# Kernel tuning notes

Hardware: AMD Instinct MI355X
Metric: run time of the kernel (lower is better)

Reference implementation:

```python
import jax, jax.numpy as jnp
import numpy as np

B, S, D = 32, 512, 512
H, DH = 8, 64          # head_num, att_embedding_size
DFF = 4 * D
NEG = float(-2**32 + 1)
LN_EPS = 1e-3          # keras LayerNormalization default


def layer_norm(x, gamma, beta):
    mu = jnp.mean(x, axis=-1, keepdims=True)
    var = jnp.mean(jnp.square(x - mu), axis=-1, keepdims=True)
    return (x - mu) / jnp.sqrt(var + LN_EPS) * gamma + beta


def setup_inputs() -> dict:
    key = jax.random.key(0)
    ks = jax.random.split(key, 10)
    queries = jax.random.normal(ks[0], (B, S, D), dtype=jnp.float32)
    keys = jax.random.normal(ks[1], (B, S, D), dtype=jnp.float32)
    query_lens = jax.random.randint(ks[2], (B, 1), 1, S + 1)
    key_lens = jax.random.randint(ks[3], (B, 1), 1, S + 1)
    # learned params (TruncatedNormal stddev 0.05-ish / Glorot approximated by scaled normals)
    W_Q = jax.random.normal(ks[4], (D, D), dtype=jnp.float32) * 0.05
    W_K = jax.random.normal(ks[5], (D, D), dtype=jnp.float32) * 0.05
    W_V = jax.random.normal(ks[6], (D, D), dtype=jnp.float32) * 0.05
    fw1 = jax.random.normal(ks[7], (D, DFF), dtype=jnp.float32) * (1.0 / np.sqrt(D))
    fw2 = jax.random.normal(ks[8], (DFF, D), dtype=jnp.float32) * (1.0 / np.sqrt(DFF))
    ln_gamma = jnp.ones((D,), dtype=jnp.float32)
    ln_beta = jnp.zeros((D,), dtype=jnp.float32)
    return {"queries": queries, "keys": keys, "W_Q": W_Q, "W_K": W_K, "W_V": W_V,
            "fw1": fw1, "fw2": fw2, "ln_gamma": ln_gamma, "ln_beta": ln_beta,
            "query_lens": query_lens, "key_lens": key_lens}


def reference(queries, keys, W_Q, W_K, W_V, fw1, fw2, ln_gamma, ln_beta, query_lens, key_lens):
    # masks from sequence lengths: [B, S] float {0,1}
    pos = jnp.arange(S)
    q_mask = (pos[None, :] < query_lens).astype(queries.dtype)  # [B,S]
    k_mask = (pos[None, :] < key_lens).astype(queries.dtype)    # [B,S]

    # QKV projections, split into heads: [B,S,H,DH]
    Q = (queries @ W_Q).reshape(B, S, H, DH)
    Kp = (keys @ W_K).reshape(B, S, H, DH)
    V = (keys @ W_V).reshape(B, S, H, DH)

    # scaled dot-product scores: [B,H,Sq,Sk]
    scores = jnp.einsum('bqhd,bkhd->bhqk', Q, Kp) / jnp.sqrt(jnp.asarray(DH, queries.dtype))

    # key padding mask
    scores = jnp.where(k_mask[:, None, None, :] == 1, scores, NEG)
    # blinding: kill the diagonal (self-position)
    eye = jnp.eye(S, dtype=bool)
    scores = jnp.where(eye[None, None, :, :], NEG, scores)

    scores = scores - jnp.max(scores, axis=-1, keepdims=True)
    attn = jax.nn.softmax(scores, axis=-1)
    # query mask zeros out padded query rows (after softmax, as in source)
    attn = attn * q_mask[:, None, :, None]

    out = jnp.einsum('bhqk,bkhd->bqhd', attn, V).reshape(B, S, D)

    result = out + queries                       # use_res
    result = layer_norm(result, ln_gamma, ln_beta)  # shared ln (use_layer_norm)

    # feed-forward
    h = jax.nn.relu(result @ fw1) @ fw2
    result = result + h
    result = layer_norm(result, ln_gamma, ln_beta)

    # output_type == 'mean'
    return jnp.mean(result, axis=1, keepdims=True)  # [B,1,D]
```

## Files before the change

kernel.cpp:

```cpp
#include <hip/hip_runtime.h>

typedef unsigned short ushort_t;
typedef unsigned int uint_t;
typedef __attribute__((ext_vector_type(4))) float f32x4;
typedef __attribute__((ext_vector_type(2))) float f32x2;
typedef __attribute__((ext_vector_type(8))) short s16x8;
typedef __attribute__((ext_vector_type(8))) _Float16 f16x8;
typedef __attribute__((ext_vector_type(4))) unsigned short u16x4;

#define NEGV -60000.0f

__device__ __forceinline__ ushort_t f2bf(float f) {
  unsigned int u = __builtin_bit_cast(unsigned int, f);
  return (ushort_t)((u + 0x7fffu + ((u >> 16) & 1u)) >> 16);
}
__device__ __forceinline__ float bf2f(ushort_t h) {
  unsigned int u = ((unsigned int)h) << 16;
  return __builtin_bit_cast(float, u);
}
__device__ __forceinline__ void gload_lds16(const void* g, void* l) {
  __builtin_amdgcn_global_load_lds(
      (const __attribute__((address_space(1))) unsigned int*)g,
      (__attribute__((address_space(3))) unsigned int*)l, 16, 0, 0);
}

template<int EPI>
__global__ __launch_bounds__(512, 2)
void gemm256(const ushort_t* __restrict__ A, const ushort_t* __restrict__ A2,
             int lda,
             const ushort_t* __restrict__ Bt, int ldb,
             void* __restrict__ Cv, int ldc, int K,
             long long sB, long long sC)
{
  __shared__ ushort_t Asm[2][16384];
  __shared__ ushort_t Bsm[2][16384];

  const int tid = threadIdx.x, wid = tid >> 6, lane = tid & 63;
  const int wr = wid >> 2, wc = wid & 3;
  const int fr = lane & 15, fq = lane >> 4;
  const int z = blockIdx.z;

  const ushort_t* Az = (z == 0) ? A : A2;
  const ushort_t* Bz = Bt + (size_t)z * sB;

  const int orig = blockIdx.x + gridDim.x * blockIdx.y;
  const int bx = (orig >> 3) % gridDim.x;
  const int by = (orig & 7) + 8 * ((orig >> 3) / gridDim.x);
  const int m0 = by * 256, n0 = bx * 256;

  const int rr0 = tid >> 3;
  const int ks = (((tid & 7) ^ (rr0 & 7)) * 8);

  auto stageA = [&](int p, int kt, int h) {
    const ushort_t* s = Az + (size_t)(m0 + h * 128 + rr0) * lda + kt * 64 + ks;
    ushort_t* d = &Asm[p][h * 8192 + tid * 8];
    gload_lds16(s, d);
    gload_lds16(s + (size_t)64 * lda, d + 4096);
  };
  auto stageB = [&](int p, int kt, int h) {
    const ushort_t* s = Bz + (size_t)(n0 + h * 128 + rr0) * ldb + kt * 64 + ks;
    ushort_t* d = &Bsm[p][h * 8192 + tid * 8];
    gload_lds16(s, d);
    gload_lds16(s + (size_t)64 * ldb, d + 4096);
  };
  auto ldA = [&](int p, int mi, int kc) -> s16x8 {
    const int R = wr * 128 + mi * 16 + fr;
    return *(const s16x8*)(&Asm[p][R * 64 + (((kc * 4 + fq) ^ (fr & 7)) * 8)]);
  };
  auto ldB = [&](int p, int ni, int kc) -> s16x8 {
    const int R = wc * 64 + ni * 16 + fr;
    return *(const s16x8*)(&Bsm[p][R * 64 + (((kc * 4 + fq) ^ (fr & 7)) * 8)]);
  };

  f32x4 acc[8][4];
#pragma unroll
  for (int m = 0; m < 8; ++m)
#pragma unroll
    for (int n = 0; n < 4; ++n)
      acc[m][n] = (f32x4){0.f, 0.f, 0.f, 0.f};

  const int nk = K >> 6;
  const int niter = nk >> 1;

  stageB(0, 0, 0); stageB(0, 0, 1);
  stageA(0, 0, 0); stageA(0, 0, 1);
  stageA(1, 1, 0); stageA(1, 1, 1);
  stageB(1, 1, 0); stageB(1, 1, 1);
  asm volatile("s_waitcnt vmcnt(8)" ::: "memory");
  __builtin_amdgcn_s_barrier();

  s16x8 af[4][2], bf[4][2];

  for (int it = 0; it < niter; ++it) {
    const int T = 2 * it;
    const bool more = (it + 1 < niter);

#pragma unroll
    for (int mi = 0; mi < 4; ++mi)
#pragma unroll
      for (int kc = 0; kc < 2; ++kc) af[mi][kc] = ldA(0, mi, kc);
#pragma unroll
    for (int ni = 0; ni < 4; ++ni)
#pragma unroll
      for (int kc = 0; kc < 2; ++kc) bf[ni][kc] = ldB(0, ni, kc);
    if (it) { stageA(1, T + 1, 0); stageA(1, T + 1, 1); }
    __builtin_amdgcn_s_barrier();
    asm volatile("s_waitcnt lgkmcnt(0)" ::: "memory");
    __builtin_amdgcn_s_setprio(1);
#pragma unroll
    for (int mi = 0; mi < 4; ++mi)
#pragma unroll
      for (int ni = 0; ni < 4; ++ni)
#pragma unroll
        for (int kc = 0; kc < 2; ++kc)
          acc[mi][ni] = __builtin_amdgcn_mfma_f32_16x16x32_bf16(
              af[mi][kc], bf[ni][kc], acc[mi][ni], 0, 0, 0);
    __builtin_amdgcn_s_setprio(0);
    __builtin_amdgcn_s_barrier();

#pragma unroll
    for (int mi = 0; mi < 4; ++mi)
#pragma unroll
      for (int kc = 0; kc < 2; ++kc) af[mi][kc] = ldA(0, 4 + mi, kc);
    if (more) {
      stageB(0, T + 2, 0); stageB(0, T + 2, 1);
      asm volatile("s_waitcnt vmcnt(4)" ::: "memory");
    } else {
      asm volatile("s_waitcnt vmcnt(0)" ::: "memory");
    }
    __builtin_amdgcn_s_barrier();
    asm volatile("s_waitcnt lgkmcnt(0)" ::: "memory");
    __builtin_amdgcn_s_setprio(1);
#pragma unroll
    for (int mi = 0; mi < 4; ++mi)
#pragma unroll
      for (int ni = 0; ni < 4; ++ni)
#pragma unroll
        for (int kc = 0; kc < 2; ++kc)
          acc[4 + mi][ni] = __builtin_amdgcn_mfma_f32_16x16x32_bf16(
              af[mi][kc], bf[ni][kc], acc[4 + mi][ni], 0, 0, 0);
    __builtin_amdgcn_s_setprio(0);
    __builtin_amdgcn_s_barrier();

#pragma unroll
    for (int mi = 0; mi < 4; ++mi)
#pragma unroll
      for (int kc = 0; kc < 2; ++kc) af[mi][kc] = ldA(1, mi, kc);
#pragma unroll
    for (int ni = 0; ni < 4; ++ni)
#pragma unroll
      for (int kc = 0; kc < 2; ++kc) bf[ni][kc] = ldB(1, ni, kc);
    if (more) { stageA(0, T + 2, 0); stageA(0, T + 2, 1); }
    __builtin_amdgcn_s_barrier();
    asm volatile("s_waitcnt lgkmcnt(0)" ::: "memory");
    __builtin_amdgcn_s_setprio(1);
#pragma unroll
    for (int mi = 0; mi < 4; ++mi)
#pragma unroll
      for (int ni = 0; ni < 4; ++ni)
#pragma unroll
        for (int kc = 0; kc < 2; ++kc)
          acc[mi][ni] = __builtin_amdgcn_mfma_f32_16x16x32_bf16(
              af[mi][kc], bf[ni][kc], acc[mi][ni], 0, 0, 0);
    __builtin_amdgcn_s_setprio(0);
    __builtin_amdgcn_s_barrier();

#pragma unroll
    for (int mi = 0; mi < 4; ++mi)
#pragma unroll
      for (int kc = 0; kc < 2; ++kc) af[mi][kc] = ldA(1, 4 + mi, kc);
    if (more) {
      stageB(1, T + 3, 0); stageB(1, T + 3, 1);
      asm volatile("s_waitcnt vmcnt(4)" ::: "memory");
    } else {
      asm volatile("s_waitcnt vmcnt(0)" ::: "memory");
    }
    __builtin_amdgcn_s_barrier();
    asm volatile("s_waitcnt lgkmcnt(0)" ::: "memory");
    __builtin_amdgcn_s_setprio(1);
#pragma unroll
    for (int mi = 0; mi < 4; ++mi)
#pragma unroll
      for (int ni = 0; ni < 4; ++ni)
#pragma unroll
        for (int kc = 0; kc < 2; ++kc)
          acc[4 + mi][ni] = __builtin_amdgcn_mfma_f32_16x16x32_bf16(
              af[mi][kc], bf[ni][kc], acc[4 + mi][ni], 0, 0, 0);
    __builtin_amdgcn_s_setprio(0);
    __builtin_amdgcn_s_barrier();
  }

  const float s0 = (EPI == 4 && z == 0) ? 0.125f : 1.0f;
  char* Cz = (char*)Cv + (size_t)sC * z;
  const int rb = fq * 4;
#pragma unroll
  for (int mi = 0; mi < 8; ++mi)
#pragma unroll
    for (int ni = 0; ni < 4; ++ni)
#pragma unroll
      for (int j = 0; j < 4; ++j) {
        const int rg = m0 + wr * 128 + mi * 16 + rb + j;
        const int cg = n0 + wc * 64 + ni * 16 + fr;
        float v = acc[mi][ni][j];
        const size_t idx = (size_t)rg * ldc + cg;
        if constexpr (EPI == 0) {
          ((float*)Cz)[idx] = v;
        } else if constexpr (EPI == 2) {
          ((ushort_t*)Cz)[idx] = f2bf(fmaxf(v, 0.f));
        } else {
          ((ushort_t*)Cz)[idx] = f2bf(v * s0);
        }
      }
}

__global__ __launch_bounds__(256)
void prep(const float* __restrict__ q, const float* __restrict__ k,
          ushort_t* __restrict__ XQ, ushort_t* __restrict__ XK,
          const float* __restrict__ W_Q, const float* __restrict__ W_K,
          const float* __restrict__ W_V,
          const float* __restrict__ fw1, const float* __restrict__ fw2,
          ushort_t* __restrict__ WQT, ushort_t* __restrict__ FW1T,
          ushort_t* __restrict__ FW2T)
{
  __shared__ float tile[32][33];
  int bid = blockIdx.x;
  if (bid < 16384) {
    const float* in = (bid < 8192) ? q : k;
    ushort_t* outp = (bid < 8192) ? XQ : XK;
    int i = (bid & 8191) * 256 + threadIdx.x;
    f32x4 v = ((const f32x4*)in)[i];
    u16x4 o;
#pragma unroll
    for (int j = 0; j < 4; ++j) o[j] = f2bf(v[j]);
    ((u16x4*)outp)[i] = o;
    return;
  }
  bid -= 16384;
  const float* in;
  ushort_t* outp;
  int R, C, bx, by;
  if (bid < 768) {
    int zz = bid >> 8, idx = bid & 255;
    in = (zz == 0) ? W_Q : (zz == 1) ? W_K : W_V;
    outp = WQT + zz * 262144;
    R = 512; C = 512; bx = idx & 15; by = idx >> 4;
  } else if (bid < 1792) {
    int idx = bid - 768;
    in = fw1; outp = FW1T; R = 512; C = 2048; bx = idx & 63; by = idx >> 6;
  } else {
    int idx = bid - 1792;
    in = fw2; outp = FW2T; R = 2048; C = 512; bx = idx & 15; by = idx >> 4;
  }
  const int c0 = bx * 32, r0 = by * 32;
  const int tx = threadIdx.x & 31, ty = threadIdx.x >> 5;
#pragma unroll
  for (int i = 0; i < 32; i += 8)
    tile[ty + i][tx] = in[(size_t)(r0 + ty + i) * C + (c0 + tx)];
  __syncthreads();
#pragma unroll
  for (int i = 0; i < 32; i += 8)
    outp[(size_t)(c0 + ty + i) * R + (r0 + tx)] = f2bf(tile[tx][ty + i]);
}

__global__ __launch_bounds__(256, 4)
void flash_attn(const ushort_t* __restrict__ Qg, const ushort_t* __restrict__ Kg,
                const ushort_t* __restrict__ Vt, ushort_t* __restrict__ AOb,
                const int* __restrict__ qlen, const int* __restrict__ klen)
{
  __shared__ ushort_t sm[20480];
  ushort_t* PQ = sm + 16384;

  const int tid = threadIdx.x, w = tid >> 6, lane = tid & 63;
  const int fr = lane & 15, fq = lane >> 4;

  int id = blockIdx.x;
  id = (id & 7) * 256 + (id >> 3);
  const int qt = id & 7, h = (id >> 3) & 7, b = id >> 6;
  const int q0 = qt * 64;
  const int KL = klen[b], QL = qlen[b];

  if (q0 >= QL) {
#pragma unroll
    for (int i = 0; i < 4; ++i) {
      int idx = i * 256 + tid;
      int rr = idx >> 4, cc = (idx & 15) << 2;
      *(u16x4*)&AOb[((size_t)(b * 512 + q0 + rr)) * 512 + h * 64 + cc] =
          (u16x4){0, 0, 0, 0};
    }
    return;
  }

  int nt = (KL + 63) >> 6;
  if (KL == 1) nt = 8;

  const ushort_t* Qrow = Qg + ((size_t)(b * 512 + q0)) * 512 + h * 64;
  const ushort_t* Krow = Kg + ((size_t)b * 512) * 512 + h * 64;
  const ushort_t* Vrow = Vt + (((size_t)b * 8 + h) * 64) * 512;

#pragma unroll
  for (int i = 0; i < 2; ++i) {
    int s = i * 256 + tid, r = s >> 3, c = (s & 7) ^ (r & 7);
    gload_lds16(Qrow + (size_t)r * 512 + c * 8, PQ + (i * 256 + w * 64) * 8);
  }
#pragma unroll
  for (int i = 0; i < 2; ++i) {
    int s = i * 256 + tid, r = s >> 3, c = (s & 7) ^ (r & 7);
    gload_lds16(Krow + (size_t)r * 512 + c * 8, sm + (i * 256 + w * 64) * 8);
    gload_lds16(Vrow + (size_t)r * 512 + c * 8, sm + 4096 + (i * 256 + w * 64) * 8);
  }
  __syncthreads();

  s16x8 qf[2];
#pragma unroll
  for (int kc = 0; kc < 2; ++kc) {
    int r = w * 16 + fr;
    qf[kc] = *(const s16x8*)(PQ + r * 64 + (((kc * 4 + fq) ^ (r & 7)) * 8));
  }

  float mrun[4], lrun[4];
  f32x4 oacc[4];
#pragma unroll
  for (int j = 0; j < 4; ++j) { mrun[j] = -1e30f; lrun[j] = 0.f; }
#pragma unroll
  for (int nd = 0; nd < 4; ++nd) oacc[nd] = (f32x4){0.f, 0.f, 0.f, 0.f};

  for (int t = 0; t < nt; ++t) {
    ushort_t* Kb = sm + (t & 1) * 8192;
    ushort_t* Vb = Kb + 4096;
    if (t + 1 < nt) {
      const int kv1 = (t + 1) * 64;
      ushort_t* Kn = sm + ((t + 1) & 1) * 8192;
#pragma unroll
      for (int i = 0; i < 2; ++i) {
        int s = i * 256 + tid, r = s >> 3, c = (s & 7) ^ (r & 7);
        gload_lds16(Krow + (size_t)(kv1 + r) * 512 + c * 8,
                    Kn + (i * 256 + w * 64) * 8);
        gload_lds16(Vrow + (size_t)r * 512 + kv1 + c * 8,
                    Kn + 4096 + (i * 256 + w * 64) * 8);
      }
    }
    const int kv0 = t * 64;

    f32x4 sacc[4];
#pragma unroll
    for (int n = 0; n < 4; ++n) sacc[n] = (f32x4){0.f, 0.f, 0.f, 0.f};
#pragma unroll
    for (int n = 0; n < 4; ++n)
#pragma unroll
      for (int kc = 0; kc < 2; ++kc) {
        int r = n * 16 + fr;
        s16x8 kf = *(const s16x8*)(Kb + r * 64 + (((kc * 4 + fq) ^ (r & 7)) * 8));
        sacc[n] = __builtin_amdgcn_mfma_f32_16x16x32_bf16(qf[kc], kf, sacc[n], 0, 0, 0);
      }

#pragma unroll
    for (int j = 0; j < 4; ++j) {
      const int rl = w * 16 + fq * 4 + j;
      const int rg = q0 + rl;
      float sv[4];
      float tmax = -1e30f;
#pragma unroll
      for (int n = 0; n < 4; ++n) {
        int cg = kv0 + n * 16 + fr;
        float v = sacc[n][j];
        if (cg >= KL || cg == rg) v = NEGV;
        sv[n] = v;
        tmax = fmaxf(tmax, v);
      }
#pragma unroll
      for (int o = 1; o < 16; o <<= 1) tmax = fmaxf(tmax, __shfl_xor(tmax, o));
      const float mnew = fmaxf(mrun[j], tmax);
      const float sf = __expf(mrun[j] - mnew);
      mrun[j] = mnew;
      float ps = 0.f;
      _Float16* prow = (_Float16*)(PQ + rl * 64);
#pragma unroll
      for (int n = 0; n < 4; ++n) {
        float p = __expf(sv[n] - mnew);
        ps += p;
        int cl = n * 2 + (fr >> 3);
        prow[((cl ^ (rl & 7)) * 8) + (fr & 7)] = (_Float16)p;
      }
      lrun[j] = lrun[j] * sf + ps;
#pragma unroll
      for (int nd = 0; nd < 4; ++nd) oacc[nd][j] *= sf;
    }

#pragma unroll
    for (int kc = 0; kc < 2; ++kc) {
      const int rl = w * 16 + fr;
      s16x8 pf = *(const s16x8*)(PQ + rl * 64 + (((kc * 4 + fq) ^ (rl & 7)) * 8));
#pragma unroll
      for (int nd = 0; nd < 4; ++nd) {
        int d = nd * 16 + fr;
        s16x8 vf = *(const s16x8*)(Vb + d * 64 + (((kc * 4 + fq) ^ (d & 7)) * 8));
        oacc[nd] = __builtin_amdgcn_mfma_f32_16x16x32_f16(
            __builtin_bit_cast(f16x8, pf), __builtin_bit_cast(f16x8, vf),
            oacc[nd], 0, 0, 0);
      }
    }
    __syncthreads();
  }

#pragma unroll
  for (int j = 0; j < 4; ++j) {
    float l = lrun[j];
#pragma unroll
    for (int o = 1; o < 16; o <<= 1) l += __shfl_xor(l, o);
    const int rg = q0 + w * 16 + fq * 4 + j;
    const float inv = (rg < QL) ? (1.f / l) : 0.f;
#pragma unroll
    for (int nd = 0; nd < 4; ++nd)
      AOb[((size_t)(b * 512 + rg)) * 512 + h * 64 + nd * 16 + fr] =
          f2bf(oacc[nd][j] * inv);
  }
}

__global__ __launch_bounds__(256) void build_vt(const ushort_t* __restrict__ V,
                                                ushort_t* __restrict__ Vt) {
  __shared__ ushort_t tile[64 * 65];
  const int s0 = blockIdx.x * 64, h = blockIdx.y, b = blockIdx.z;
  const int t = threadIdx.x;
#pragma unroll
  for (int i = 0; i < 16; ++i) {
    int idx = i * 256 + t;
    int sl = idx >> 6, d = idx & 63;
    tile[sl * 65 + d] = V[(size_t)(b * 512 + s0 + sl) * 512 + h * 64 + d];
  }
  __syncthreads();
  _Float16* vt = (_Float16*)Vt;
#pragma unroll
  for (int i = 0; i < 16; ++i) {
    int idx = i * 256 + t;
    int d = idx >> 6, sl = idx & 63;
    vt[((size_t)(b * 8 + h) * 64 + d) * 512 + (s0 + sl)] =
        (_Float16)bf2f(tile[sl * 65 + d]);
  }
}

__global__ __launch_bounds__(256) void ln1(const ushort_t* __restrict__ xb,
                                           const float* __restrict__ r,
                                           const float* __restrict__ g,
                                           const float* __restrict__ be,
                                           ushort_t* __restrict__ ob) {
  const int row = blockIdx.x, t = threadIdx.x;
  const size_t base = (size_t)row * 512;
  const uint_t xv = ((const uint_t*)(xb + base))[t];
  const f32x2 rv = ((const f32x2*)(r + base))[t];
  float v0 = bf2f((ushort_t)(xv & 0xffff)) + rv[0];
  float v1 = bf2f((ushort_t)(xv >> 16)) + rv[1];
  float s = v0 + v1, q = v0 * v0 + v1 * v1;
#pragma unroll
  for (int o = 32; o; o >>= 1) { s += __shfl_xor(s, o); q += __shfl_xor(q, o); }
  __shared__ float ps[4], pq[4];
  const int w = t >> 6, lane = t & 63;
  if (lane == 0) { ps[w] = s; pq[w] = q; }
  __syncthreads();
  s = ps[0] + ps[1] + ps[2] + ps[3];
  q = pq[0] + pq[1] + pq[2] + pq[3];
  const float mu = s * 0.001953125f;
  const float var = q * 0.001953125f - mu * mu;
  const float inv = 1.0f / sqrtf(var + 1e-3f);
  const float y0 = (v0 - mu) * inv * g[2 * t] + be[2 * t];
  const float y1 = (v1 - mu) * inv * g[2 * t + 1] + be[2 * t + 1];
  ((uint_t*)(ob + base))[t] = (uint_t)f2bf(y0) | ((uint_t)f2bf(y1) << 16);
}

__global__ __launch_bounds__(256) void ln2(const float* __restrict__ h2a,
                                           const float* __restrict__ h2b,
                                           const ushort_t* __restrict__ r1b,
                                           const float* __restrict__ g,
                                           const float* __restrict__ be,
                                           ushort_t* __restrict__ ob) {
  const int row = blockIdx.x, t = threadIdx.x;
  const size_t base = (size_t)row * 512;
  const f32x2 a = ((const f32x2*)(h2a + base))[t];
  const f32x2 b = ((const f32x2*)(h2b + base))[t];
  const uint_t rv = ((const uint_t*)(r1b + base))[t];
  float v0 = a[0] + b[0] + bf2f((ushort_t)(rv & 0xffff));
  float v1 = a[1] + b[1] + bf2f((ushort_t)(rv >> 16));
  float s = v0 + v1, q = v0 * v0 + v1 * v1;
#pragma unroll
  for (int o = 32; o; o >>= 1) { s += __shfl_xor(s, o); q += __shfl_xor(q, o); }
  __shared__ float ps[4], pq[4];
  const int w = t >> 6, lane = t & 63;
  if (lane == 0) { ps[w] = s; pq[w] = q; }
  __syncthreads();
  s = ps[0] + ps[1] + ps[2] + ps[3];
  q = pq[0] + pq[1] + pq[2] + pq[3];
  const float mu = s * 0.001953125f;
  const float var = q * 0.001953125f - mu * mu;
  const float inv = 1.0f / sqrtf(var + 1e-3f);
  const float y0 = (v0 - mu) * inv * g[2 * t] + be[2 * t];
  const float y1 = (v1 - mu) * inv * g[2 * t + 1] + be[2 * t + 1];
  ((uint_t*)(ob + base))[t] = (uint_t)f2bf(y0) | ((uint_t)f2bf(y1) << 16);
}

__global__ void mean_partial(const ushort_t* __restrict__ r3,
                             float* __restrict__ part) {
  const int sc = blockIdx.x, b = blockIdx.y, d = threadIdx.x;
  float s = 0.f;
#pragma unroll 4
  for (int i = 0; i < 64; ++i)
    s += bf2f(r3[(size_t)(b * 512 + sc * 64 + i) * 512 + d]);
  part[(size_t)(b * 8 + sc) * 512 + d] = s;
}
__global__ void mean_final(const float* __restrict__ part, float* __restrict__ out) {
  const int b = blockIdx.x, d = threadIdx.x;
  float s = 0.f;
#pragma unroll
  for (int i = 0; i < 8; ++i) s += part[(size_t)(b * 8 + i) * 512 + d];
  out[b * 512 + d] = s * (1.0f / 512.0f);
}

extern "C" void kernel_launch(void* const* d_in, const int* in_sizes, int n_in,
                              void* d_out, int out_size, void* d_ws, size_t ws_size,
                              hipStream_t stream) {
  (void)in_sizes; (void)n_in; (void)out_size; (void)ws_size;
  const float* queries = (const float*)d_in[0];
  const float* keys    = (const float*)d_in[1];
  const float* W_Q = (const float*)d_in[2];
  const float* W_K = (const float*)d_in[3];
  const float* W_V = (const float*)d_in[4];
  const float* fw1 = (const float*)d_in[5];
  const float* fw2 = (const float*)d_in[6];
  const float* ln_g = (const float*)d_in[7];
  const float* ln_b = (const float*)d_in[8];
  const int* qlen = (const int*)d_in[9];
  const int* klen = (const int*)d_in[10];
  float* out = (float*)d_out;

  char* ws = (char*)d_ws;
  const size_t MB = 1048576;
  ushort_t* XQ  = (ushort_t*)(ws + 0 * MB);
  ushort_t* XK  = (ushort_t*)(ws + 16 * MB);
  ushort_t* Qb  = (ushort_t*)(ws + 32 * MB);
  ushort_t* Vb  = (ushort_t*)(ws + 64 * MB);
  ushort_t* VT  = (ushort_t*)(ws + 80 * MB);
  ushort_t* AOb = (ushort_t*)(ws + 96 * MB);
  ushort_t* R1B = (ushort_t*)(ws + 112 * MB);
  ushort_t* H1  = (ushort_t*)(ws + 0 * MB);
  float*    H2  = (float*)(ws + 128 * MB);
  ushort_t* R3B = (ushort_t*)(ws + 192 * MB);
  char*     wsw = ws + 208 * MB;
  ushort_t* WQT  = (ushort_t*)(wsw);
  ushort_t* FW1T = (ushort_t*)(wsw + 3 * 524288);
  ushort_t* FW2T = (ushort_t*)(wsw + 3 * 524288 + 2097152);
  float*    PART = (float*)(wsw + 3 * 524288 + 2 * 2097152);

  prep<<<19200, 256, 0, stream>>>(queries, keys, XQ, XK, W_Q, W_K, W_V,
                                  fw1, fw2, WQT, FW1T, FW2T);
  gemm256<4><<<dim3(2, 64, 3), 512, 0, stream>>>(
      XQ, XK, 512, WQT, 512, (void*)Qb, 512, 512, 262144, 16 * MB);
  build_vt<<<dim3(8, 8, 32), 256, 0, stream>>>(Vb, VT);
  flash_attn<<<2048, 256, 0, stream>>>(Qb, Qb + 8388608, VT, AOb, qlen, klen);
  ln1<<<16384, 256, 0, stream>>>(AOb, queries, ln_g, ln_b, R1B);
  gemm256<2><<<dim3(8, 64, 1), 512, 0, stream>>>(
      R1B, R1B, 512, FW1T, 512, (void*)H1, 2048, 512, 0, 0);
  gemm256<0><<<dim3(2, 64, 2), 512, 0, stream>>>(
      H1, H1 + 1024, 2048, FW2T, 2048, (void*)H2, 512, 1024, 1024, 32 * MB);
  ln2<<<16384, 256, 0, stream>>>(H2, H2 + 8388608, R1B, ln_g, ln_b, R3B);
  mean_partial<<<dim3(8, 32), 512, 0, stream>>>(R3B, PART);
  mean_final<<<32, 512, 0, stream>>>(PART, out);
}
```

Baseline: 233.6 us.

## Add 128x128 GEMM for QKV projection that skips padded row tiles

Result: no change. 230.1 us (-1.5%).

```diff
diff --git a/kernel.cpp b/kernel.cpp
--- a/kernel.cpp
+++ b/kernel.cpp
@@ -22,6 +22,116 @@
   __builtin_amdgcn_global_load_lds(
       (const __attribute__((address_space(1))) unsigned int*)g,
       (__attribute__((address_space(3))) unsigned int*)l, 16, 0, 0);
+}
+
+template<int EPI>
+__global__ __launch_bounds__(256)
+void gemm_bt(const ushort_t* __restrict__ A, const ushort_t* __restrict__ A2,
+             int lda,
+             const ushort_t* __restrict__ Bt, int ldb,
+             void* __restrict__ Cv, int ldc, int K,
+             long long sB, long long sC,
+             const int* __restrict__ qlen, const int* __restrict__ klen)
+{
+  __shared__ ushort_t As[2][128 * 32];
+  __shared__ ushort_t Bs[2][128 * 32];
+
+  const int tid = threadIdx.x;
+  const int w = tid >> 6;
+  const int lane = tid & 63;
+  const int z = blockIdx.z;
+
+  const ushort_t* Az = (z == 0) ? A : A2;
+  const ushort_t* Bz = Bt + (size_t)z * sB;
+
+  const int orig = blockIdx.x + gridDim.x * blockIdx.y;
+  const int bx = (orig >> 3) % gridDim.x;
+  const int by = (orig & 7) + 8 * ((orig >> 3) / gridDim.x);
+  const int m0 = by * 128;
+  const int n0 = bx * 128;
+
+  if constexpr (EPI == 4) {
+    const int s0 = m0 & 511;
+    if (s0) {
+      const int b = m0 >> 9;
+      const int L = (z == 0) ? qlen[b] : klen[b];
+      if (L <= s0 && !(z == 2 && L == 1)) return;
+    }
+  }
+
+  const int wm = (w >> 1) * 64;
+  const int wn = (w & 1) * 64;
+
+  f32x4 acc[4][4];
+#pragma unroll
+  for (int m = 0; m < 4; ++m)
+#pragma unroll
+    for (int n = 0; n < 4; ++n)
+      acc[m][n] = (f32x4){0.f, 0.f, 0.f, 0.f};
+
+  const int cA0 = w * 64 + lane;
+  const int cA1 = 256 + cA0;
+  const int rA0 = cA0 >> 2, kO0 = (cA0 & 3) * 8;
+  const int rA1 = cA1 >> 2, kO1 = (cA1 & 3) * 8;
+
+  auto stage = [&](int p, int k0) {
+    gload_lds16(Az + (size_t)(m0 + rA0) * lda + (k0 + kO0),
+                As[p] + (size_t)(w * 64) * 8);
+    gload_lds16(Az + (size_t)(m0 + rA1) * lda + (k0 + kO1),
+                As[p] + (size_t)(256 + w * 64) * 8);
+    gload_lds16(Bz + (size_t)(n0 + rA0) * ldb + (k0 + kO0),
+                Bs[p] + (size_t)(w * 64) * 8);
+    gload_lds16(Bz + (size_t)(n0 + rA1) * ldb + (k0 + kO1),
+                Bs[p] + (size_t)(256 + w * 64) * 8);
+  };
+
+  const int nk = K >> 5;
+  stage(0, 0);
+  __syncthreads();
+  for (int kt = 0; kt < nk; ++kt) {
+    const int p = kt & 1;
+    if (kt + 1 < nk) stage(p ^ 1, (kt + 1) << 5);
+
+    s16x8 af[4], bfr[4];
+#pragma unroll
+    for (int m = 0; m < 4; ++m)
+      af[m] = *(const s16x8*)(As[p] + (size_t)(wm + m * 16 + (lane & 15)) * 32 +
+                              ((lane >> 4) * 8));
+#pragma unroll
+    for (int n = 0; n < 4; ++n)
+      bfr[n] = *(const s16x8*)(Bs[p] + (size_t)(wn + n * 16 + (lane & 15)) * 32 +
+                               ((lane >> 4) * 8));
+#pragma unroll
+    for (int m = 0; m < 4; ++m)
+#pragma unroll
+      for (int n = 0; n < 4; ++n)
+        acc[m][n] = __builtin_amdgcn_mfma_f32_16x16x32_bf16(af[m], bfr[n],
+                                                            acc[m][n], 0, 0, 0);
+    __syncthreads();
+  }
+
+  const float s0v = (EPI == 4 && z == 0) ? 0.125f : 1.0f;
+  char* Cz = (char*)Cv + (size_t)sC * z;
+  const int r_base = (lane >> 4) * 4;
+  const int c_base = lane & 15;
+#pragma unroll
+  for (int m = 0; m < 4; ++m)
+#pragma unroll
+    for (int n = 0; n < 4; ++n)
+#pragma unroll
+      for (int j = 0; j < 4; ++j) {
+        const int rg = m0 + wm + m * 16 + r_base + j;
+        const int cg = n0 + wn + n * 16 + c_base;
+        float v = acc[m][n][j];
+        const size_t idx = (size_t)rg * ldc + cg;
+        if constexpr (EPI == 0) {
+          ((float*)Cz)[idx] = v;
+        } else if constexpr (EPI == 2) {
+          ((ushort_t*)Cz)[idx] = f2bf(fmaxf(v, 0.f));
+        } else {
+          ((ushort_t*)Cz)[idx] = f2bf(v * s0v);
+        }
+      }
 }
 
 template<int EPI>
@@ -550,8 +660,8 @@
 
   prep<<<19200, 256, 0, stream>>>(queries, keys, XQ, XK, W_Q, W_K, W_V,
                                   fw1, fw2, WQT, FW1T, FW2T);
-  gemm256<4><<<dim3(2, 64, 3), 512, 0, stream>>>(
-      XQ, XK, 512, WQT, 512, (void*)Qb, 512, 512, 262144, 16 * MB);
+  gemm_bt<4><<<dim3(4, 128, 3), 256, 0, stream>>>(
+      XQ, XK, 512, WQT, 512, (void*)Qb, 512, 512, 262144, 16 * MB, qlen, klen);
   build_vt<<<dim3(8, 8, 32), 256, 0, stream>>>(Vb, VT);
   flash_attn<<<2048, 256, 0, stream>>>(Qb, Qb + 8388608, VT, AOb, qlen, klen);
   ln1<<<16384, 256, 0, stream>>>(AOb, queries, ln_g, ln_b, R1B);
```
